# Optimization experiments

Measured on AMD Instinct MI355X. Metric: run time of the kernel, lower is better.

## Reference

```python
import jax, jax.numpy as jnp
import numpy as np

IN_FEATURES = 4096
OUT_FEATURES = 16384
BATCH, SEQ = 4, 2048
INT8_QMIN, INT8_QMAX = -127, 127


def setup_inputs() -> dict:
    key = jax.random.key(0)
    k_x, k_w, k_s, k_b = jax.random.split(key, 4)
    x = jax.random.normal(k_x, (BATCH, SEQ, IN_FEATURES), dtype=jnp.float32)
    # symmetric int8 quantized weights in [-127, 127]
    weight_q = jax.random.randint(k_w, (OUT_FEATURES, IN_FEATURES), INT8_QMIN, INT8_QMAX + 1, dtype=jnp.int32).astype(jnp.int8)
    # realistic per-out-channel scales (positive, small)
    scale_w = (jax.random.uniform(k_s, (OUT_FEATURES,), dtype=jnp.float32) * 0.02 + 1e-4)
    bias = jax.random.normal(k_b, (OUT_FEATURES,), dtype=jnp.float32)
    return {"x": x, "weight_q": weight_q, "scale_w": scale_w, "bias": bias}


def reference(x, weight_q, scale_w, bias):
    # Dequantize: W[o, i] = weight_q[o, i] * scale_w[o]
    W = weight_q.astype(jnp.float32) * scale_w[:, None]  # [O, I]
    # F.linear: y = x @ W^T + b
    return jnp.einsum("bsi,oi->bso", x, W) + bias
```

## Files before the change

### kernel.cpp

```cpp
#include <hip/hip_runtime.h>
#include <stdint.h>

#define K_DIM 4096
#define N_DIM 16384
#define M_DIM 8192

typedef __attribute__((ext_vector_type(8))) __bf16 bf16x8;
typedef __attribute__((ext_vector_type(4))) float f32x4;
typedef __attribute__((ext_vector_type(8))) unsigned short us8;

__device__ __forceinline__ void async_ld16(const void* g, void* l) {
    __builtin_amdgcn_global_load_lds((const __attribute__((address_space(1))) void*)g,
                                     (__attribute__((address_space(3))) void*)l, 16, 0, 0);
}

__device__ __forceinline__ unsigned short bf16_rn(float f) {
    unsigned b = __builtin_bit_cast(unsigned, f);
    return (unsigned short)((b + 0x7fffu + ((b >> 16) & 1u)) >> 16);
}

__global__ __launch_bounds__(256) void qlin_cvt_w(const int* __restrict__ wq,
                                                  unsigned short* __restrict__ w2,
                                                  int total16) {
    int idx = blockIdx.x * 256 + threadIdx.x;
    int stride = gridDim.x * 256;
    for (; idx < total16; idx += stride) {
        const int4* src = reinterpret_cast<const int4*>(wq) + (size_t)idx * 4;
        int4 a = src[0], b = src[1], c = src[2], d = src[3];
        int v[16] = {a.x, a.y, a.z, a.w, b.x, b.y, b.z, b.w,
                     c.x, c.y, c.z, c.w, d.x, d.y, d.z, d.w};
        us8 o0, o1;
#pragma unroll
        for (int e = 0; e < 8; ++e) {
            float f0 = (float)v[e];
            float f1 = (float)v[8 + e];
            o0[e] = (unsigned short)(__builtin_bit_cast(unsigned, f0) >> 16);
            o1[e] = (unsigned short)(__builtin_bit_cast(unsigned, f1) >> 16);
        }
        us8* dst = reinterpret_cast<us8*>(w2 + (size_t)idx * 16);
        dst[0] = o0; dst[1] = o1;
    }
}

__global__ __launch_bounds__(256) void qlin_cvt_a(const float* __restrict__ x,
                                                  unsigned short* __restrict__ ab,
                                                  int total8) {
    int idx = blockIdx.x * 256 + threadIdx.x;
    int stride = gridDim.x * 256;
    for (; idx < total8; idx += stride) {
        const float4* src = reinterpret_cast<const float4*>(x + (size_t)idx * 8);
        float4 v0 = src[0], v1 = src[1];
        float f[8] = {v0.x, v0.y, v0.z, v0.w, v1.x, v1.y, v1.z, v1.w};
        us8 h;
#pragma unroll
        for (int e = 0; e < 8; ++e) h[e] = bf16_rn(f[e]);
        *reinterpret_cast<us8*>(ab + (size_t)idx * 8) = h;
    }
}

__device__ __forceinline__ void tile_mfma(const unsigned short* sA, const unsigned short* sW,
                                          f32x4 (&acc)[4][4], int r, int kc, int wr, int wc) {
    bf16x8 fw[4], fa[4];
#pragma unroll
    for (int ni = 0; ni < 4; ++ni)
        fw[ni] = *reinterpret_cast<const bf16x8*>(&sW[(wc + ni * 16 + r) * 32 + kc * 8]);
#pragma unroll
    for (int mi = 0; mi < 4; ++mi)
        fa[mi] = *reinterpret_cast<const bf16x8*>(&sA[(wr + mi * 16 + r) * 32 + kc * 8]);
#pragma unroll
    for (int mi = 0; mi < 4; ++mi)
#pragma unroll
        for (int ni = 0; ni < 4; ++ni)
            acc[mi][ni] = __builtin_amdgcn_mfma_f32_16x16x32_bf16(fa[mi], fw[ni], acc[mi][ni], 0, 0, 0);
}

__device__ __forceinline__ void epilogue(f32x4 (&acc)[4][4], const float* __restrict__ scale,
                                         const float* __restrict__ bias, float* __restrict__ out,
                                         int bm, int bn, int wr, int wc, int lane) {
    int r = lane & 15, rq = (lane >> 4) * 4;
#pragma unroll
    for (int ni = 0; ni < 4; ++ni) {
        int c = bn + wc + ni * 16 + r;
        float s = scale[c], bb = bias[c];
#pragma unroll
        for (int mi = 0; mi < 4; ++mi) {
            int r0 = bm + wr + mi * 16 + rq;
#pragma unroll
            for (int j = 0; j < 4; ++j)
                out[(size_t)(r0 + j) * N_DIM + c] = acc[mi][ni][j] * s + bb;
        }
    }
}

__global__ __launch_bounds__(256, 2) void qlin_gemm_fast(const unsigned short* __restrict__ Ab,
                                                         const unsigned short* __restrict__ Wt,
                                                         const float* __restrict__ scale,
                                                         const float* __restrict__ bias,
                                                         float* __restrict__ out) {
    __shared__ unsigned short sA[128 * 32], sW[128 * 32];
    const int tid = threadIdx.x;
    const int lane = tid & 63;
    const int wid = tid >> 6;
    int id2 = ((int)blockIdx.x & 7) * 1024 + ((int)blockIdx.x >> 3);
    const int bm = (id2 >> 7) * 128;
    const int bn = (id2 & 127) * 128;
    const int wr = (wid >> 1) * 64;
    const int wc = (wid & 1) * 64;

    const unsigned short* gsrc[4];
    unsigned short* ldst[4];
#pragma unroll
    for (int i = 0; i < 4; ++i) {
        int chunk = wid * 4 + i;
        int tile = chunk >> 3, c8 = chunk & 7;
        const unsigned short* src = (tile == 0) ? Ab : Wt;
        unsigned short* dst = (tile == 0) ? sA : sW;
        int rb = (tile == 0) ? bm : bn;
        int row = c8 * 16 + (lane >> 2);
        gsrc[i] = src + (size_t)(rb + row) * K_DIM + (lane & 3) * 8;
        ldst[i] = dst + c8 * 512;
    }

    f32x4 acc[4][4] = {};
    const int r = lane & 15, kc = lane >> 4;

    for (int kt = 0; kt < K_DIM / 32; ++kt) {
        __syncthreads();
#pragma unroll
        for (int i = 0; i < 4; ++i) async_ld16(gsrc[i] + (size_t)kt * 32, ldst[i]);
        __syncthreads();
        tile_mfma(sA, sW, acc, r, kc, wr, wc);
    }
    epilogue(acc, scale, bias, out, bm, bn, wr, wc, lane);
}

__global__ __launch_bounds__(256, 2) void qlin_gemm_fb(const float* __restrict__ x,
                                                       const int* __restrict__ wq,
                                                       const float* __restrict__ scale,
                                                       const float* __restrict__ bias,
                                                       float* __restrict__ out) {
    __shared__ unsigned short sA[128 * 32], sW[128 * 32];
    const int tid = threadIdx.x;
    const int lane = tid & 63;
    const int wid = tid >> 6;
    int id2 = ((int)blockIdx.x & 7) * 1024 + ((int)blockIdx.x >> 3);
    const int bm = (id2 >> 7) * 128;
    const int bn = (id2 & 127) * 128;
    const int wr = (wid >> 1) * 64;
    const int wc = (wid & 1) * 64;

    const int row = tid >> 1, half = tid & 1;
    const float* ga = x  + (size_t)(bm + row) * K_DIM + half * 16;
    const int*   gw = wq + (size_t)(bn + row) * K_DIM + half * 16;
    us8* dA = reinterpret_cast<us8*>(&sA[row * 32 + half * 16]);
    us8* dW = reinterpret_cast<us8*>(&sW[row * 32 + half * 16]);

    f32x4 acc[4][4] = {};
    const int r = lane & 15, kc = lane >> 4;

    for (int kt = 0; kt < K_DIM / 32; ++kt) {
        const float4* af = reinterpret_cast<const float4*>(ga + kt * 32);
        float4 v0 = af[0], v1 = af[1], v2 = af[2], v3 = af[3];
        const int4* wf = reinterpret_cast<const int4*>(gw + kt * 32);
        int4 w0 = wf[0], w1 = wf[1], w2 = wf[2], w3 = wf[3];
        float f[16] = {v0.x, v0.y, v0.z, v0.w, v1.x, v1.y, v1.z, v1.w,
                       v2.x, v2.y, v2.z, v2.w, v3.x, v3.y, v3.z, v3.w};
        int   q[16] = {w0.x, w0.y, w0.z, w0.w, w1.x, w1.y, w1.z, w1.w,
                       w2.x, w2.y, w2.z, w2.w, w3.x, w3.y, w3.z, w3.w};
        us8 ha[2], hw[2];
#pragma unroll
        for (int e = 0; e < 16; ++e) {
            ha[e >> 3][e & 7] = bf16_rn(f[e]);
            float wv = (float)q[e];
            hw[e >> 3][e & 7] = (unsigned short)(__builtin_bit_cast(unsigned, wv) >> 16);
        }
        __syncthreads();
        dA[0] = ha[0]; dA[1] = ha[1];
        dW[0] = hw[0]; dW[1] = hw[1];
        __syncthreads();
        tile_mfma(sA, sW, acc, r, kc, wr, wc);
    }
    epilogue(acc, scale, bias, out, bm, bn, wr, wc, lane);
}

extern "C" void kernel_launch(void* const* d_in, const int* in_sizes, int n_in,
                              void* d_out, int out_size, void* d_ws, size_t ws_size,
                              hipStream_t stream) {
    const float* x  = (const float*)d_in[0];
    const int*   wq = (const int*)d_in[1];
    const float* sw = (const float*)d_in[2];
    const float* bs = (const float*)d_in[3];
    float* out = (float*)d_out;

    const size_t need = (size_t)M_DIM * K_DIM * 2
                      + (size_t)N_DIM * K_DIM * 2;

    if (ws_size >= need) {
        unsigned short* ab = (unsigned short*)d_ws;
        unsigned short* w2 = ab + (size_t)M_DIM * K_DIM;
        qlin_cvt_a<<<2048, 256, 0, stream>>>(x, ab, (M_DIM * (K_DIM / 8)));
        qlin_cvt_w<<<2048, 256, 0, stream>>>(wq, w2, (N_DIM * (K_DIM / 16)));
        qlin_gemm_fast<<<dim3(8192), dim3(256), 0, stream>>>(ab, w2, sw, bs, out);
    } else {
        qlin_gemm_fb<<<dim3(8192), dim3(256), 0, stream>>>(x, wq, sw, bs, out);
    }
}
```

Measured before the change: 2.307 ms.

## Swizzle LDS tile layout, remap block-to-XCD tiling, raise occupancy hint

Applies an XOR swizzle to the 16-byte k-chunks in the shared-memory A/W tiles, both on the async global-to-LDS writes and on the fragment reads, to cut LDS bank conflicts. It also remaps block IDs so each XCD owns a contiguous band of N columns and iterates over all M tiles, improving L2 reuse of weight tiles per XCD. The launch-bounds occupancy hint is raised from 2 to 4 blocks per CU, which may increase register pressure or cause spills. The fallback kernel gets the same swizzle and mapping.

Result: faster. 2.196 ms (-4.8%).

```diff
diff --git a/kernel.cpp b/kernel.cpp
--- a/kernel.cpp
+++ b/kernel.cpp
@@ -59,14 +59,14 @@
 }
 
 __device__ __forceinline__ void tile_mfma(const unsigned short* sA, const unsigned short* sW,
-                                          f32x4 (&acc)[4][4], int r, int kc, int wr, int wc) {
+                                          f32x4 (&acc)[4][4], int r, int kx, int wr, int wc) {
     bf16x8 fw[4], fa[4];
 #pragma unroll
     for (int ni = 0; ni < 4; ++ni)
-        fw[ni] = *reinterpret_cast<const bf16x8*>(&sW[(wc + ni * 16 + r) * 32 + kc * 8]);
+        fw[ni] = *reinterpret_cast<const bf16x8*>(&sW[(wc + ni * 16 + r) * 32 + kx]);
 #pragma unroll
     for (int mi = 0; mi < 4; ++mi)
-        fa[mi] = *reinterpret_cast<const bf16x8*>(&sA[(wr + mi * 16 + r) * 32 + kc * 8]);
+        fa[mi] = *reinterpret_cast<const bf16x8*>(&sA[(wr + mi * 16 + r) * 32 + kx]);
 #pragma unroll
     for (int mi = 0; mi < 4; ++mi)
 #pragma unroll
@@ -92,7 +92,7 @@
     }
 }
 
-__global__ __launch_bounds__(256, 2) void qlin_gemm_fast(const unsigned short* __restrict__ Ab,
+__global__ __launch_bounds__(256, 4) void qlin_gemm_fast(const unsigned short* __restrict__ Ab,
                                                          const unsigned short* __restrict__ Wt,
                                                          const float* __restrict__ scale,
                                                          const float* __restrict__ bias,
@@ -101,9 +101,10 @@
     const int tid = threadIdx.x;
     const int lane = tid & 63;
     const int wid = tid >> 6;
-    int id2 = ((int)blockIdx.x & 7) * 1024 + ((int)blockIdx.x >> 3);
-    const int bm = (id2 >> 7) * 128;
-    const int bn = (id2 & 127) * 128;
+    const int xcd = (int)blockIdx.x & 7;
+    const int j   = (int)blockIdx.x >> 3;
+    const int bn  = (xcd * 16 + (j >> 6)) * 128;
+    const int bm  = (j & 63) * 128;
     const int wr = (wid >> 1) * 64;
     const int wc = (wid & 1) * 64;
 
@@ -117,19 +118,22 @@
         unsigned short* dst = (tile == 0) ? sA : sW;
         int rb = (tile == 0) ? bm : bn;
         int row = c8 * 16 + (lane >> 2);
-        gsrc[i] = src + (size_t)(rb + row) * K_DIM + (lane & 3) * 8;
+        int ci  = (lane & 3) ^ ((lane >> 3) & 3);
+        gsrc[i] = src + (size_t)(rb + row) * K_DIM + ci * 8;
         ldst[i] = dst + c8 * 512;
     }
 
     f32x4 acc[4][4] = {};
-    const int r = lane & 15, kc = lane >> 4;
+    const int r = lane & 15;
+    const int kc = lane >> 4;
+    const int kx = (kc ^ ((r >> 1) & 3)) * 8;
 
     for (int kt = 0; kt < K_DIM / 32; ++kt) {
         __syncthreads();
 #pragma unroll
         for (int i = 0; i < 4; ++i) async_ld16(gsrc[i] + (size_t)kt * 32, ldst[i]);
         __syncthreads();
-        tile_mfma(sA, sW, acc, r, kc, wr, wc);
+        tile_mfma(sA, sW, acc, r, kx, wr, wc);
     }
     epilogue(acc, scale, bias, out, bm, bn, wr, wc, lane);
 }
@@ -143,20 +147,24 @@
     const int tid = threadIdx.x;
     const int lane = tid & 63;
     const int wid = tid >> 6;
-    int id2 = ((int)blockIdx.x & 7) * 1024 + ((int)blockIdx.x >> 3);
-    const int bm = (id2 >> 7) * 128;
-    const int bn = (id2 & 127) * 128;
+    const int xcd = (int)blockIdx.x & 7;
+    const int j   = (int)blockIdx.x >> 3;
+    const int bn  = (xcd * 16 + (j >> 6)) * 128;
+    const int bm  = (j & 63) * 128;
     const int wr = (wid >> 1) * 64;
     const int wc = (wid & 1) * 64;
 
     const int row = tid >> 1, half = tid & 1;
     const float* ga = x  + (size_t)(bm + row) * K_DIM + half * 16;
     const int*   gw = wq + (size_t)(bn + row) * K_DIM + half * 16;
-    us8* dA = reinterpret_cast<us8*>(&sA[row * 32 + half * 16]);
-    us8* dW = reinterpret_cast<us8*>(&sW[row * 32 + half * 16]);
+    const int x2 = (row >> 1) & 3;
+    us8* bA = reinterpret_cast<us8*>(&sA[row * 32]);
+    us8* bW = reinterpret_cast<us8*>(&sW[row * 32]);
 
     f32x4 acc[4][4] = {};
-    const int r = lane & 15, kc = lane >> 4;
+    const int r = lane & 15;
+    const int kc = lane >> 4;
+    const int kx = (kc ^ ((r >> 1) & 3)) * 8;
 
     for (int kt = 0; kt < K_DIM / 32; ++kt) {
         const float4* af = reinterpret_cast<const float4*>(ga + kt * 32);
@@ -175,10 +183,12 @@
             hw[e >> 3][e & 7] = (unsigned short)(__builtin_bit_cast(unsigned, wv) >> 16);
         }
         __syncthreads();
-        dA[0] = ha[0]; dA[1] = ha[1];
-        dW[0] = hw[0]; dW[1] = hw[1];
-        __syncthreads();
-        tile_mfma(sA, sW, acc, r, kc, wr, wc);
+        bA[(half * 2 + 0) ^ x2] = ha[0];
+        bA[(half * 2 + 1) ^ x2] = ha[1];
+        bW[(half * 2 + 0) ^ x2] = hw[0];
+        bW[(half * 2 + 1) ^ x2] = hw[1];
+        __syncthreads();
+        tile_mfma(sA, sW, acc, r, kx, wr, wc);
     }
     epilogue(acc, scale, bias, out, bm, bn, wr, wc, lane);
 }
```
